# Optimization experiments

Measured on AMD Instinct MI355X. Metric: run time of the kernel, lower is better.

The kernel has to match this reference:

```python
import jax, jax.numpy as jnp
import numpy as np

B, S, D, A, C, TT, T, NS = 64, 512, 1024, 128, 64, 32, 40, 64
NEG = -1e9


def setup_inputs() -> dict:
    key = jax.random.key(0)
    ks = jax.random.split(key, 24)
    n = lambda k, sh, s: jax.random.normal(k, sh, dtype=jnp.float32) * s
    inp = {
        "encoded_src": n(ks[0], (B, S, D), 1.0),
        "encoded_col": n(ks[1], (B, C, D), 1.0),
        "encoded_tab": n(ks[2], (B, TT, D), 1.0),
        "h0": n(ks[3], (B, D), 1.0),
        "c0": n(ks[4], (B, D), 1.0),
        "action_emb": n(ks[5], (A, D), 0.1),
        "symbol_emb": n(ks[6], (NS, D), 0.1),
        "W_tgt": n(ks[7], (D, D), 0.02), "b_tgt": jnp.zeros((D,), jnp.float32),
        "W_act": n(ks[8], (D, D), 0.02), "b_act": jnp.zeros((D,), jnp.float32),
        "W_col": n(ks[9], (D, D), 0.02), "b_col": jnp.zeros((D,), jnp.float32),
        "W_tab": n(ks[10], (D, D), 0.02), "b_tab": jnp.zeros((D,), jnp.float32),
        "W_out": n(ks[11], (D, D), 0.02), "b_out": jnp.zeros((D,), jnp.float32),
        "W_ih": n(ks[12], (3 * D, 4 * D), 0.02), "b_ih": jnp.zeros((4 * D,), jnp.float32),
        "W_hh": n(ks[13], (D, 4 * D), 0.02), "b_hh": jnp.zeros((4 * D,), jnp.float32),
        "src_mask": jnp.zeros((B, S), jnp.int32),
        "col_mask": jnp.zeros((B, C), jnp.int32),
        "tab_mask": jnp.zeros((B, TT), jnp.int32),
        "action_mask": jnp.zeros((B, A), jnp.int32),
        "cur_node_ids": jax.random.randint(ks[14], (T, B), 0, NS, dtype=jnp.int32),
        "kind": jax.random.randint(ks[15], (T, B), 0, 3, dtype=jnp.int32),
        "gold_idx": jax.random.randint(ks[16], (T, B), 0, TT, dtype=jnp.int32),
    }
    return inp


def reference(encoded_src, encoded_col, encoded_tab, h0, c0, action_emb, symbol_emb,
              W_tgt, b_tgt, W_act, b_act, W_col, b_col, W_tab, b_tab, W_out, b_out,
              W_ih, b_ih, W_hh, b_hh,
              src_mask, col_mask, tab_mask, action_mask, cur_node_ids, kind, gold_idx):
    dt = encoded_src.dtype
    nT, nB = cur_node_ids.shape
    nA = action_emb.shape[0]
    nC = encoded_col.shape[1]
    nTT = encoded_tab.shape[1]
    dim = encoded_src.shape[-1]

    # mask==1 means masked-out (matches torch code: allowed positions set to 0)
    src_bias = jnp.where(src_mask == 1, NEG, 0.0).astype(dt)
    act_bias = jnp.where(action_mask == 1, NEG, 0.0).astype(dt)
    col_bias = jnp.where(col_mask == 1, NEG, 0.0).astype(dt)
    tab_bias = jnp.where(tab_mask == 1, NEG, 0.0).astype(dt)

    # previous-action embedding per step: gather from action table / encoded cols / encoded tabs
    bidx = jnp.arange(nB)
    prev_a = action_emb[gold_idx % nA]                       # [T,B,D]
    prev_c = encoded_col[bidx[None, :], gold_idx % nC]       # [T,B,D]
    prev_t = encoded_tab[bidx[None, :], gold_idx % nTT]      # [T,B,D]
    k3 = kind[..., None]
    prev_sel = jnp.where(k3 == 0, prev_a, jnp.where(k3 == 1, prev_c, prev_t))
    # step 0 uses a zero prev-action embedding
    prev_emb = jnp.concatenate([jnp.zeros((1, nB, dim), dt), prev_sel[:-1]], axis=0)
    node_emb = symbol_emb[cur_node_ids]                      # [T,B,D]

    def step(carry, xs):
        h, c, loss = carry
        pe, ne, kd, gi = xs
        # attention over encoded_src using affine(h) as query
        q = h @ W_tgt + b_tgt                                            # [B,D]
        att = jax.nn.softmax(jnp.einsum('bsd,bd->bs', encoded_src, q) + src_bias, axis=-1)
        ctx = jnp.einsum('bs,bsd->bd', att, encoded_src)                 # [B,D]
        # LSTMCell
        x = jnp.concatenate([pe, ne, ctx], axis=-1)                      # [B,3D]
        gates = x @ W_ih + b_ih + h @ W_hh + b_hh                        # [B,4D]
        i, f, g, o = jnp.split(gates, 4, axis=-1)
        c2 = jax.nn.sigmoid(f) * c + jax.nn.sigmoid(i) * jnp.tanh(g)
        h2 = jax.nn.sigmoid(o) * jnp.tanh(c2)
        out = h2 @ W_out + b_out                                         # [B,D]
        # three prediction heads (action / column / table views)
        la = jax.nn.log_softmax(jnp.einsum('ad,bd->ba', action_emb, out @ W_act + b_act) + act_bias, axis=-1)
        lc = jax.nn.log_softmax(jnp.einsum('bcd,bd->bc', encoded_col, out @ W_col + b_col) + col_bias, axis=-1)
        lt = jax.nn.log_softmax(jnp.einsum('btd,bd->bt', encoded_tab, out @ W_tab + b_tab) + tab_bias, axis=-1)
        ga = jnp.take_along_axis(la, (gi % nA)[:, None], 1)[:, 0]
        gc = jnp.take_along_axis(lc, (gi % nC)[:, None], 1)[:, 0]
        gt = jnp.take_along_axis(lt, (gi % nTT)[:, None], 1)[:, 0]
        lp = jnp.where(kd == 0, ga, jnp.where(kd == 1, gc, gt))
        return (h2, c2, loss - lp), None

    (h, c, loss), _ = jax.lax.scan(step, (h0, c0, jnp.zeros((nB,), dt)),
                                   (prev_emb, node_emb, kind, gold_idx))
    return loss
```

## Files before the change

kernel.cpp:

```cpp
#include <hip/hip_runtime.h>
#include <math.h>

typedef short s8v __attribute__((ext_vector_type(8)));
typedef __bf16 bf8 __attribute__((ext_vector_type(8)));
typedef float f4v __attribute__((ext_vector_type(4)));

#define DEV static __device__ __forceinline__

DEV ushort f2bf(float f){
  union { float f; unsigned u; } v; v.f = f;
  unsigned u = v.u;
  return (ushort)((u + 0x7fffu + ((u>>16)&1u)) >> 16);
}
DEV float bf2f(ushort u){
  union { unsigned u; float f; } v; v.u = ((unsigned)u)<<16; return v.f;
}
DEV float sigm(float x){ return 1.0f/(1.0f + __expf(-x)); }
DEV float tanh_(float x){ float e=__expf(2.f*x); return 1.f - 2.f/(e+1.f); }
DEV float wred(float x){
  #pragma unroll
  for(int off=32; off; off>>=1) x += __shfl_xor(x, off, 64);
  return x;
}
DEV int swz(int row, int uscol){
  return (row<<6) + ((((uscol>>3) ^ (row&7))<<3) | (uscol&7));
}
DEV void gload16(const void* g, void* l){
  __builtin_amdgcn_global_load_lds((const __attribute__((address_space(1))) void*)g,
                                   (__attribute__((address_space(3))) void*)l, 16, 0, 0);
}
DEV int gperm(int n){
  return (((n&1023)>>4)<<6) | ((n>>10)<<4) | (n&15);
}


__global__ void k_cast(const float* __restrict__ s, ushort* __restrict__ d, long n4){
  long i = (long)blockIdx.x*256 + threadIdx.x;
  const long st = (long)gridDim.x*256;
  for(; i<n4; i+=st){
    float4 v = ((const float4*)s)[i];
    ushort4 o; o.x=f2bf(v.x); o.y=f2bf(v.y); o.z=f2bf(v.z); o.w=f2bf(v.w);
    ((ushort4*)d)[i]=o;
  }
}

__global__ __launch_bounds__(256) void k_tr7(const float* __restrict__ wih,
    const float* __restrict__ whh, const float* __restrict__ wtgt,
    const float* __restrict__ wcol, const float* __restrict__ wtab,
    const float* __restrict__ wact, ushort* __restrict__ WihT,
    ushort* __restrict__ WcatT, ushort* __restrict__ WtgtT, ushort* __restrict__ BcatT)
{
  __shared__ ushort T[64][72];
  const int bid = blockIdx.x;
  const float* src; ushort* dst; int C, ldd, roff, cx, ry; bool pm;
  if(bid < 2048){ src=wih; C=4096; dst=WihT; ldd=2048; roff=0; cx=bid&63; ry=bid>>6; pm=true; }
  else if(bid < 3072){ int j=bid-2048; src=wih+2048L*4096; C=4096; dst=WcatT; ldd=2048; roff=0; cx=j&63; ry=j>>6; pm=true; }
  else if(bid < 4096){ int j=bid-3072; src=whh; C=4096; dst=WcatT; ldd=2048; roff=1024; cx=j&63; ry=j>>6; pm=true; }
  else if(bid < 4352){ int j=bid-4096; src=wtgt; C=1024; dst=WtgtT; ldd=1024; roff=0; cx=j&15; ry=j>>4; pm=false; }
  else if(bid < 4608){ int j=bid-4352; src=wcol; C=1024; dst=BcatT; ldd=1024; roff=0; cx=j&15; ry=j>>4; pm=false; }
  else if(bid < 4864){ int j=bid-4608; src=wtab; C=1024; dst=BcatT+1048576; ldd=1024; roff=0; cx=j&15; ry=j>>4; pm=false; }
  else { int j=bid-4864; src=wact; C=1024; dst=BcatT+2097152; ldd=1024; roff=0; cx=j&15; ry=j>>4; pm=false; }
  const int c0 = cx<<6, r0 = ry<<6;
  const int tid = threadIdx.x;
  {
    const int rr = tid>>2, cc = (tid&3)<<4;
    const float* s = src + (long)(r0+rr)*C + c0 + cc;
    float4 v0=*(const float4*)(s), v1=*(const float4*)(s+4), v2=*(const float4*)(s+8), v3=*(const float4*)(s+12);
    ushort* t = &T[rr][cc];
    t[0]=f2bf(v0.x); t[1]=f2bf(v0.y); t[2]=f2bf(v0.z); t[3]=f2bf(v0.w);
    t[4]=f2bf(v1.x); t[5]=f2bf(v1.y); t[6]=f2bf(v1.z); t[7]=f2bf(v1.w);
    t[8]=f2bf(v2.x); t[9]=f2bf(v2.y); t[10]=f2bf(v2.z); t[11]=f2bf(v2.w);
    t[12]=f2bf(v3.x); t[13]=f2bf(v3.y); t[14]=f2bf(v3.z); t[15]=f2bf(v3.w);
  }
  __syncthreads();
  {
    const int rr = tid>>2, cc = (tid&3)<<4;
    s8v o0, o1;
    #pragma unroll
    for(int i=0;i<8;i++){ o0[i]=(short)T[cc+i][rr]; o1[i]=(short)T[cc+8+i][rr]; }
    const int n = c0 + rr;
    const int nr = pm ? gperm(n) : n;
    ushort* dp = dst + (long)nr*ldd + roff + r0 + cc;
    *(s8v*)dp = o0; *(s8v*)(dp+8) = o1;
  }
}

__global__ void k_gatherP(const float* __restrict__ emba, const float* __restrict__ ecol,
                          const float* __restrict__ etab, const float* __restrict__ symb,
                          const int* __restrict__ kindv, const int* __restrict__ gold,
                          const int* __restrict__ cur, ushort* __restrict__ P){
  long i = (long)blockIdx.x*256 + threadIdx.x;
  const long st = (long)gridDim.x*256;
  const long n4 = 2560L*2048/4;
  for(; i<n4; i+=st){
    long pos = i*4; int row = (int)(pos>>11); int col = (int)(pos&2047);
    int t = row>>6, b = row&63;
    ushort4 o;
    if(col < 1024){
      if(t==0){ o.x=o.y=o.z=o.w=0; *(ushort4*)&P[pos]=o; continue; }
      int k = kindv[(t-1)*64+b];
      int gi = gold[(t-1)*64+b];
      const float* s;
      if(k==0) s = emba + ((long)(gi & 127))*1024 + col;
      else if(k==1) s = ecol + (((long)b<<6) + (gi & 63))*1024 + col;
      else s = etab + (((long)b<<5) + (gi & 31))*1024 + col;
      float4 v = *(const float4*)s;
      o.x=f2bf(v.x); o.y=f2bf(v.y); o.z=f2bf(v.z); o.w=f2bf(v.w);
    } else {
      const float* s = symb + ((long)cur[t*64+b])*1024 + (col-1024);
      float4 v = *(const float4*)s;
      o.x=f2bf(v.x); o.y=f2bf(v.y); o.z=f2bf(v.z); o.w=f2bf(v.w);
    }
    *(ushort4*)&P[pos] = o;
  }
}

__global__ void k_init(const float* __restrict__ h0, const float* __restrict__ c0,
                       const float* __restrict__ bih, const float* __restrict__ bhh,
                       const int* __restrict__ smask,
                       float* __restrict__ cbuf, ushort* __restrict__ Ab0,
                       float* __restrict__ biasvec, float* __restrict__ sbias){
  int i = blockIdx.x*256 + threadIdx.x;
  if(i < 65536){
    cbuf[i]=c0[i];
    int row=i>>10, col=i&1023;
    Ab0[(row<<11)+1024+col]=f2bf(h0[i]);
  }
  if(i < 32768) sbias[i] = (smask[i]==1) ? -1.0e9f : 0.f;
  if(i < 4096){
    int nt=i>>6, g=(i>>4)&3, j16=i&15;
    int n = (g<<10) | (nt<<4) | j16;
    biasvec[i] = bih[n] + bhh[n];
  }
}

__global__ void k_bias1(const float* __restrict__ bout,
                        const float* __restrict__ Wa, const float* __restrict__ ba,
                        const float* __restrict__ Wc, const float* __restrict__ bc,
                        const float* __restrict__ Wt, const float* __restrict__ bt,
                        float* __restrict__ vv){
  int j = blockIdx.x*256 + threadIdx.x;
  if(j >= 3072) return;
  int which = j>>10, col = j&1023;
  const float* W = (which==0)?Wa:(which==1)?Wc:Wt;
  const float* bb = (which==0)?ba:(which==1)?bc:bt;
  float s = bb[col];
  for(int i=0;i<1024;i++) s += bout[i]*W[((long)i<<10)+col];
  vv[j] = s;
}

__global__ void k_bias2a(const float* __restrict__ vv, const float* __restrict__ emb,
                         const float* __restrict__ ecol, const float* __restrict__ etab,
                         float* __restrict__ dbuf){
  int wid = blockIdx.x*4 + (threadIdx.x>>6);
  int l = threadIdx.x & 63;
  if(wid >= 6272) return;
  const float* src; const float* v;
  if(wid < 128){ src = emb + ((long)wid<<10); v = vv; }
  else if(wid < 4224){ src = ecol + ((long)(wid-128)<<10); v = vv+1024; }
  else { src = etab + ((long)(wid-4224)<<10); v = vv+2048; }
  const float* sp = src + l*16; const float* vp = v + l*16;
  float s = 0.f;
  #pragma unroll
  for(int i=0;i<16;i+=4){
    float4 a = *(const float4*)(sp+i); float4 bvv = *(const float4*)(vp+i);
    s += a.x*bvv.x + a.y*bvv.y + a.z*bvv.z + a.w*bvv.w;
  }
  s = wred(s);
  if(l==0) dbuf[wid] = s;
}

__global__ void k_bias2b(const float* __restrict__ dbuf,
                         const int* __restrict__ amask, const int* __restrict__ cmask,
                         const int* __restrict__ tmask,
                         float* __restrict__ ca, float* __restrict__ cb, float* __restrict__ ct){
  int i = blockIdx.x*256 + threadIdx.x;
  if(i < 8192){ ca[i] = dbuf[i&127] + ((amask[i]==1)?-1.0e9f:0.f); }
  else if(i < 12288){ int j=i-8192; cb[j] = dbuf[128+j] + ((cmask[j]==1)?-1.0e9f:0.f); }
  else if(i < 14336){ int j=i-12288; ct[j] = dbuf[4224+j] + ((tmask[j]==1)?-1.0e9f:0.f); }
}

template<bool OBF16, bool HASB>
__global__ __launch_bounds__(256,2) void k_gemm128(const ushort* __restrict__ Ap,
    const ushort* __restrict__ Bp, void* __restrict__ Cp, const float* __restrict__ bias,
    int N, int K)
{
  __shared__ __align__(16) ushort As[2][8192];
  __shared__ __align__(16) ushort Bs[2][8192];
  const int tid=threadIdx.x, w=tid>>6, l=tid&63;
  const int wr=w>>1, wc=w&1;
  const int m0=blockIdx.y<<7, n0=blockIdx.x<<7;
  const int lr8 = l>>3, lc = l&7;
  f4v acc[4][4];
  #pragma unroll
  for(int m=0;m<4;m++)
    #pragma unroll
    for(int n=0;n<4;n++) acc[m][n]=(f4v){0.f,0.f,0.f,0.f};

  auto stage=[&](int buf, int k0){
    #pragma unroll
    for(int i=0;i<4;i++){
      const int rb = i*32 + w*8;
      const int row = rb + lr8;
      const int cp = (lc ^ (row&7))<<3;
      gload16(Ap + (long)(m0+row)*K + k0 + cp, &As[buf][rb<<6]);
      gload16(Bp + (long)(n0+row)*K + k0 + cp, &Bs[buf][rb<<6]);
    }
  };
  auto compute=[&](int buf){
    #pragma unroll
    for(int ks=0; ks<2; ks++){
      bf8 av[4], bv[4];
      #pragma unroll
      for(int m=0;m<4;m++){
        const int ar = wr*64 + (m<<4) + (l&15);
        const int ch = (ks<<2) + (l>>4);
        av[m] = *(const bf8*)&As[buf][(ar<<6) + ((ch ^ (ar&7))<<3)];
      }
      #pragma unroll
      for(int n=0;n<4;n++){
        const int br = wc*64 + (n<<4) + (l&15);
        const int ch = (ks<<2) + (l>>4);
        bv[n] = *(const bf8*)&Bs[buf][(br<<6) + ((ch ^ (br&7))<<3)];
      }
      #pragma unroll
      for(int m=0;m<4;m++)
        #pragma unroll
        for(int n=0;n<4;n++)
          acc[m][n] = __builtin_amdgcn_mfma_f32_16x16x32_bf16(av[m], bv[n], acc[m][n], 0,0,0);
    }
  };

  stage(0, 0);
  asm volatile("s_waitcnt vmcnt(0)" ::: "memory");
  __syncthreads();
  int cur=0;
  for(int k0=0;;){
    const int kn = k0+64;
    if(kn<K) stage(cur^1, kn);
    compute(cur);
    asm volatile("s_waitcnt vmcnt(0)" ::: "memory");
    __syncthreads();
    if(kn>=K) break;
    k0=kn; cur^=1;
  }
  #pragma unroll
  for(int m=0;m<4;m++){
    #pragma unroll
    for(int n=0;n<4;n++){
      const int col = n0 + wc*64 + (n<<4) + (l&15);
      float bv_ = 0.f;
      if constexpr(HASB) bv_ = bias[col];
      #pragma unroll
      for(int j=0;j<4;j++){
        const int row = m0 + wr*64 + (m<<4) + ((l>>4)<<2) + j;
        float v = acc[m][n][j] + bv_;
        if constexpr(OBF16) ((ushort*)Cp)[(long)row*N + col] = f2bf(v);
        else ((float*)Cp)[(long)row*N + col] = v;
      }
    }
  }
}

template<bool AF32, bool OBF16, bool HASB>
__global__ __launch_bounds__(256) void k_gemm(const void* __restrict__ Ap,
    const ushort* __restrict__ Bp, void* __restrict__ Cp, const float* __restrict__ bias,
    int M, int N, int K, int lda, int ldb, int ldc, long sAz, long sCz)
{
  __shared__ __align__(16) ushort As[4096];
  __shared__ __align__(16) ushort Bs[4096];
  const int tid=threadIdx.x, w=tid>>6, l=tid&63, q4=l>>4;
  const int r=tid>>2, cc=(tid&3)<<4;
  const int m0=blockIdx.y<<6, n0=blockIdx.x<<6;
  const int z=blockIdx.z;
  f4v acc[4];
  #pragma unroll
  for(int i=0;i<4;i++) acc[i]=(f4v){0.f,0.f,0.f,0.f};

  struct PF { float4 f0,f1,f2,f3; s8v u0,u1,b0,b1; };
  PF pA, pB;

  auto loadAB=[&](int k0, PF& p){
    const int gm = m0 + r;
    if constexpr(AF32){
      if(gm < M){
        const float* a = (const float*)Ap + sAz*z + (long)gm*lda + k0 + cc;
        p.f0=*(const float4*)(a); p.f1=*(const float4*)(a+4); p.f2=*(const float4*)(a+8); p.f3=*(const float4*)(a+12);
      } else { p.f0=p.f1=p.f2=p.f3=make_float4(0.f,0.f,0.f,0.f); }
    } else {
      if(gm < M){
        const ushort* a = (const ushort*)Ap + sAz*z + (long)gm*lda + k0 + cc;
        p.u0=*(const s8v*)a; p.u1=*(const s8v*)(a+8);
      } else { p.u0=p.u1=(s8v){0,0,0,0,0,0,0,0}; }
    }
    const ushort* b = Bp + (long)(n0+r)*ldb + k0 + cc;
    p.b0=*(const s8v*)b; p.b1=*(const s8v*)(b+8);
  };
  auto stage=[&](const PF& p){
    s8v a0, a1;
    if constexpr(AF32){
      a0[0]=(short)f2bf(p.f0.x); a0[1]=(short)f2bf(p.f0.y); a0[2]=(short)f2bf(p.f0.z); a0[3]=(short)f2bf(p.f0.w);
      a0[4]=(short)f2bf(p.f1.x); a0[5]=(short)f2bf(p.f1.y); a0[6]=(short)f2bf(p.f1.z); a0[7]=(short)f2bf(p.f1.w);
      a1[0]=(short)f2bf(p.f2.x); a1[1]=(short)f2bf(p.f2.y); a1[2]=(short)f2bf(p.f2.z); a1[3]=(short)f2bf(p.f2.w);
      a1[4]=(short)f2bf(p.f3.x); a1[5]=(short)f2bf(p.f3.y); a1[6]=(short)f2bf(p.f3.z); a1[7]=(short)f2bf(p.f3.w);
    } else { a0=p.u0; a1=p.u1; }
    *(s8v*)&As[swz(r,cc)] = a0; *(s8v*)&As[swz(r,cc+8)] = a1;
    *(s8v*)&Bs[swz(r,cc)] = p.b0; *(s8v*)&Bs[swz(r,cc+8)] = p.b1;
  };
  auto compute=[&](){
    #pragma unroll
    for(int ks=0; ks<64; ks+=32){
      bf8 av = *(const bf8*)&As[swz((w<<4)+(l&15), ks+(q4<<3))];
      #pragma unroll
      for(int nf=0; nf<4; nf++){
        bf8 bv = *(const bf8*)&Bs[swz((nf<<4)+(l&15), ks+(q4<<3))];
        acc[nf] = __builtin_amdgcn_mfma_f32_16x16x32_bf16(av, bv, acc[nf], 0, 0, 0);
      }
    }
  };

  loadAB(0, pA); loadAB(64, pB);
  for(int k0=0; k0<K; k0+=128){
    stage(pA); __syncthreads();
    if(k0+128 < K) loadAB(k0+128, pA);
    compute(); __syncthreads();
    stage(pB); __syncthreads();
    if(k0+192 < K) loadAB(k0+192, pB);
    compute(); __syncthreads();
  }
  #pragma unroll
  for(int nf=0; nf<4; nf++){
    const int col = n0 + (nf<<4) + (l&15);
    float bv = 0.f;
    if constexpr(HASB) bv = bias[col];
    #pragma unroll
    for(int j=0;j<4;j++){
      const int row = m0 + (w<<4) + ((l>>4)<<2) + j;
      if(row < M){
        float v = acc[nf][j] + bv;
        if constexpr(OBF16) ((ushort*)Cp)[sCz*z + (long)row*ldc + col] = f2bf(v);
        else ((float*)Cp)[sCz*z + (long)row*ldc + col] = v;
      }
    }
  }
}


__global__ __launch_bounds__(256) void k_attn(const ushort* __restrict__ esrc,
    const float* __restrict__ q, const float* __restrict__ sbias,
    float* __restrict__ pm, float* __restrict__ pl, float* __restrict__ pctx)
{
  const int b = blockIdx.x>>4, j = blockIdx.x&15;
  const int tid = threadIdx.x, w = tid>>6, l = tid&63;
  __shared__ float ms[4], ls[4];
  __shared__ float ctxs[4][1024];
  float qr[16];
  {
    const float* qp = q + (b<<10) + (l<<4);
    #pragma unroll
    for(int i=0;i<16;i+=4){ float4 v=*(const float4*)(qp+i); qr[i]=v.x; qr[i+1]=v.y; qr[i+2]=v.z; qr[i+3]=v.w; }
  }
  float m = -3.4e38f, lsum = 0.f;
  float cacc[16];
  #pragma unroll
  for(int i=0;i<16;i++) cacc[i]=0.f;
  const int sbase = (j<<5) + w;
  for(int rr=0; rr<8; rr++){
    const int s = sbase + (rr<<2);
    const ushort* ep = esrc + (((long)((b<<9) + s))<<10) + (l<<4);
    s8v e0 = *(const s8v*)ep, e1 = *(const s8v*)(ep+8);
    float ef[16];
    #pragma unroll
    for(int i=0;i<8;i++){ ef[i]=bf2f((ushort)e0[i]); ef[8+i]=bf2f((ushort)e1[i]); }
    float d = 0.f;
    #pragma unroll
    for(int i=0;i<16;i++) d += ef[i]*qr[i];
    d = wred(d);
    d += sbias[(b<<9)+s];
    const float mn = fmaxf(m, d);
    const float sc = __expf(m - mn);
    const float p = __expf(d - mn);
    lsum = lsum*sc + p;
    #pragma unroll
    for(int i=0;i<16;i++) cacc[i] = cacc[i]*sc + p*ef[i];
    m = mn;
  }
  if(l==0){ ms[w]=m; ls[w]=lsum; }
  #pragma unroll
  for(int i=0;i<16;i++) ctxs[w][(l<<4)+i]=cacc[i];
  __syncthreads();
  const float mb = fmaxf(fmaxf(ms[0],ms[1]),fmaxf(ms[2],ms[3]));
  const float w0=__expf(ms[0]-mb), w1=__expf(ms[1]-mb), w2=__expf(ms[2]-mb), w3=__expf(ms[3]-mb);
  const float lb = ls[0]*w0 + ls[1]*w1 + ls[2]*w2 + ls[3]*w3;
  const int jb = (j<<6) + b;
  float* pc = pctx + ((long)jb<<10);
  for(int d0=tid; d0<1024; d0+=256){
    pc[d0] = ctxs[0][d0]*w0 + ctxs[1][d0]*w1 + ctxs[2][d0]*w2 + ctxs[3][d0]*w3;
  }
  if(tid==0){ pm[jb]=mb; pl[jb]=lb; }
}

__global__ __launch_bounds__(256) void k_combine(const float* __restrict__ pm,
    const float* __restrict__ pl, const float* __restrict__ pctx, ushort* __restrict__ Ab)
{
  const int idx = blockIdx.x*256 + threadIdx.x;
  const int b = idx>>7, c0 = (idx&127)<<3;
  float mv[16];
  #pragma unroll
  for(int j=0;j<16;j++) mv[j] = pm[(j<<6)+b];
  float M = mv[0];
  #pragma unroll
  for(int j=1;j<16;j++) M = fmaxf(M, mv[j]);
  float e[16]; float den = 0.f;
  #pragma unroll
  for(int j=0;j<16;j++){ e[j] = __expf(mv[j]-M); den += pl[(j<<6)+b]*e[j]; }
  const float inv = 1.f/den;
  float s0=0,s1=0,s2=0,s3=0,s4=0,s5=0,s6=0,s7=0;
  #pragma unroll
  for(int j=0;j<16;j++){
    const float wj = e[j]*inv;
    const float* p = pctx + (((long)((j<<6)+b))<<10) + c0;
    float4 v0=*(const float4*)p, v1=*(const float4*)(p+4);
    s0+=wj*v0.x; s1+=wj*v0.y; s2+=wj*v0.z; s3+=wj*v0.w;
    s4+=wj*v1.x; s5+=wj*v1.y; s6+=wj*v1.z; s7+=wj*v1.w;
  }
  s8v o;
  o[0]=(short)f2bf(s0); o[1]=(short)f2bf(s1); o[2]=(short)f2bf(s2); o[3]=(short)f2bf(s3);
  o[4]=(short)f2bf(s4); o[5]=(short)f2bf(s5); o[6]=(short)f2bf(s6); o[7]=(short)f2bf(s7);
  *(s8v*)&Ab[(b<<11)+c0] = o;
}

__global__ __launch_bounds__(256) void k_lstm(const ushort* __restrict__ Abuf,
    const float* __restrict__ cin, const ushort* __restrict__ WcatP,
    const ushort* __restrict__ gpre_t, float* __restrict__ cout,
    ushort* __restrict__ AbOut, ushort* __restrict__ h2t)
{
  __shared__ __align__(16) ushort As[4096];
  __shared__ __align__(16) ushort Bs[4096];
  const int tid=threadIdx.x, w=tid>>6, l=tid&63, q4=l>>4, l15=l&15;
  const int r=tid>>2, cc=(tid&3)<<4;
  const int nt = blockIdx.x;
  f4v acc[4];
  #pragma unroll
  for(int nf=0;nf<4;nf++){
    #pragma unroll
    for(int jj=0;jj<4;jj++){
      const int row = (w<<4) + ((l>>4)<<2) + jj;
      acc[nf][jj] = bf2f(gpre_t[((long)row<<12) + (nt<<6) + (nf<<4) + l15]);
    }
  }
  struct PF { s8v a0,a1,b0,b1; };
  PF pA, pB;
  auto loadAB=[&](int k0, PF& p){
    const ushort* a = Abuf + ((long)r<<11) + k0 + cc;
    p.a0=*(const s8v*)a; p.a1=*(const s8v*)(a+8);
    const ushort* bp = WcatP + ((long)((nt<<6)+r)<<11) + k0 + cc;
    p.b0=*(const s8v*)bp; p.b1=*(const s8v*)(bp+8);
  };
  auto stage=[&](const PF& p){
    *(s8v*)&As[swz(r,cc)] = p.a0; *(s8v*)&As[swz(r,cc+8)] = p.a1;
    *(s8v*)&Bs[swz(r,cc)] = p.b0; *(s8v*)&Bs[swz(r,cc+8)] = p.b1;
  };
  auto compute=[&](){
    #pragma unroll
    for(int ks=0; ks<64; ks+=32){
      bf8 av = *(const bf8*)&As[swz((w<<4)+l15, ks+(q4<<3))];
      #pragma unroll
      for(int nf=0;nf<4;nf++){
        bf8 bv = *(const bf8*)&Bs[swz((nf<<4)+l15, ks+(q4<<3))];
        acc[nf] = __builtin_amdgcn_mfma_f32_16x16x32_bf16(av, bv, acc[nf], 0, 0, 0);
      }
    }
  };
  loadAB(0, pA); loadAB(64, pB);
  for(int k0=0; k0<2048; k0+=128){
    stage(pA); __syncthreads();
    if(k0+128 < 2048) loadAB(k0+128, pA);
    compute(); __syncthreads();
    stage(pB); __syncthreads();
    if(k0+192 < 2048) loadAB(k0+192, pB);
    compute(); __syncthreads();
  }
  #pragma unroll
  for(int jj=0;jj<4;jj++){
    const int row = (w<<4) + ((l>>4)<<2) + jj;
    const int j = (nt<<4) + l15;
    const float iv = acc[0][jj], fv = acc[1][jj], gv = acc[2][jj], ov = acc[3][jj];
    const float cold = cin[(row<<10)+j];
    const float c2 = sigm(fv)*cold + sigm(iv)*tanh_(gv);
    const float h2v = sigm(ov)*tanh_(c2);
    cout[(row<<10)+j] = c2;
    const ushort hb = f2bf(h2v);
    AbOut[(row<<11) + 1024 + j] = hb;
    h2t[(row<<10)+j] = hb;
  }
}

__global__ __launch_bounds__(256) void k_loss(const ushort* __restrict__ h2a,
    const ushort* __restrict__ GAt, const ushort* __restrict__ GCt, const ushort* __restrict__ GTt,
    const float* __restrict__ ca, const float* __restrict__ cb, const float* __restrict__ ct,
    const int* __restrict__ gold, const int* __restrict__ kindv, float* __restrict__ lossbuf)
{
  const int blk = blockIdx.x;
  const int t = blk/192, rem = blk - t*192;
  const int b = rem/3, head = rem - b*3;
  const int tid = threadIdx.x, w = tid>>6, l = tid&63;
  __shared__ float logits[128];
  int R; const ushort* G; const float* cons;
  if(head==0){ R=128; G=GAt; cons=ca + (b<<7); }
  else if(head==1){ R=64; G=GCt + ((long)b<<16); cons=cb + (b<<6); }
  else { R=32; G=GTt + ((long)b<<15); cons=ct + (b<<5); }
  float hr[16];
  {
    const ushort* hp = h2a + (((long)((t<<6)+b))<<10) + l*16;
    s8v h0v=*(const s8v*)hp, h1v=*(const s8v*)(hp+8);
    #pragma unroll
    for(int i=0;i<8;i++){ hr[i]=bf2f((ushort)h0v[i]); hr[8+i]=bf2f((ushort)h1v[i]); }
  }
  for(int rr=w; rr<R; rr+=4){
    const ushort* gp = G + ((long)rr<<10) + l*16;
    s8v g0=*(const s8v*)gp, g1=*(const s8v*)(gp+8);
    float d = 0.f;
    #pragma unroll
    for(int i=0;i<8;i++){ d += bf2f((ushort)g0[i])*hr[i]; d += bf2f((ushort)g1[i])*hr[8+i]; }
    d = wred(d);
    if(l==0) logits[rr] = d + cons[rr];
  }
  __syncthreads();
  if(w==0){
    float mx = -3.4e38f;
    for(int idx=l; idx<R; idx+=64) mx = fmaxf(mx, logits[idx]);
    #pragma unroll
    for(int off=32; off; off>>=1) mx = fmaxf(mx, __shfl_xor(mx, off, 64));
    float s = 0.f;
    for(int idx=l; idx<R; idx+=64) s += __expf(logits[idx]-mx);
    s = wred(s);
    if(l==0){
      const float lse = mx + __logf(s);
      const int kd = kindv[(t<<6)+b];
      const bool mine = (head==0 && kd==0) || (head==1 && kd==1) || (head==2 && kd>=2);
      if(mine){
        const int gi = gold[(t<<6)+b];
        lossbuf[(t<<6)+b] = logits[gi & (R-1)] - lse;
      }
    }
  }
}

__global__ void k_loss_fin(const float* __restrict__ lossbuf, float* __restrict__ out){
  int b = threadIdx.x;
  if(b < 64){
    float s = 0.f;
    for(int t=0;t<40;t++) s += lossbuf[(t<<6)+b];
    out[b] = -s;
  }
}


extern "C" void kernel_launch(void* const* d_in, const int* in_sizes, int n_in,
                              void* d_out, int out_size, void* d_ws, size_t ws_size,
                              hipStream_t stream)
{
  const float *e_src=(const float*)d_in[0], *e_col=(const float*)d_in[1], *e_tab=(const float*)d_in[2];
  const float *h0=(const float*)d_in[3], *c0=(const float*)d_in[4];
  const float *emba=(const float*)d_in[5], *embs=(const float*)d_in[6];
  const float *W_tgt=(const float*)d_in[7], *b_tgt=(const float*)d_in[8];
  const float *W_act=(const float*)d_in[9], *b_act=(const float*)d_in[10];
  const float *W_col=(const float*)d_in[11], *b_col=(const float*)d_in[12];
  const float *W_tab=(const float*)d_in[13], *b_tab=(const float*)d_in[14];
  const float *W_out=(const float*)d_in[15], *b_out=(const float*)d_in[16];
  const float *W_ih=(const float*)d_in[17], *b_ih=(const float*)d_in[18];
  const float *W_hh=(const float*)d_in[19], *b_hh=(const float*)d_in[20];
  const int *smask=(const int*)d_in[21], *cmask=(const int*)d_in[22], *tmask=(const int*)d_in[23];
  const int *amask=(const int*)d_in[24];
  const int *cur=(const int*)d_in[25], *kindp=(const int*)d_in[26], *goldp=(const int*)d_in[27];

  char* wp = (char*)d_ws;
  auto alloc = [&](size_t n)->char*{ char* p = wp; wp += (n + 255) & ~(size_t)255; return p; };
  ushort* esrc_bf = (ushort*)alloc(67108864);
  ushort* WihT    = (ushort*)alloc(16777216);
  ushort* WcatP   = (ushort*)alloc(16777216);
  ushort* WtgtT   = (ushort*)alloc(2097152);
  ushort* BcatT   = (ushort*)alloc(6291456);
  ushort* Woutb   = (ushort*)alloc(2097152);
  float*  U       = (float*) alloc(12582912);
  ushort* Ubf     = (ushort*)alloc(6291456);
  ushort* GAt     = (ushort*)alloc(262144);
  ushort* GCt     = (ushort*)alloc(8388608);
  ushort* GTt     = (ushort*)alloc(4194304);
  ushort* gpre    = (ushort*)alloc(20971520);
  float* biasvec  = (float*)alloc(16384);
  float* sbias    = (float*)alloc(131072);
  float* vv       = (float*)alloc(12288);
  float* dbuf     = (float*)alloc(25088);
  float* ca       = (float*)alloc(32768);
  float* cb       = (float*)alloc(16384);
  float* ctb      = (float*)alloc(8192);
  float* pm       = (float*)alloc(4096);
  float* pl       = (float*)alloc(4096);
  float* pctx     = (float*)alloc(4194304);
  ushort* Ab0     = (ushort*)alloc(262144);
  ushort* Ab1     = (ushort*)alloc(262144);
  float* cbuf0    = (float*)alloc(262144);
  float* cbuf1    = (float*)alloc(262144);
  float* qb       = (float*)alloc(262144);
  ushort* h2a     = (ushort*)alloc(5242880);
  float* lossbuf  = (float*)alloc(10240);
  ushort* P       = (ushort*)U;
  float* out      = (float*)d_out;

  k_cast<<<4096,256,0,stream>>>(e_src, esrc_bf, 8388608L);
  k_cast<<<512,256,0,stream>>>(W_out, Woutb, 262144L);
  k_tr7<<<5120,256,0,stream>>>(W_ih, W_hh, W_tgt, W_col, W_tab, W_act,
                               WihT, WcatP, WtgtT, BcatT);
  k_init<<<256,256,0,stream>>>(h0, c0, b_ih, b_hh, smask, cbuf0, Ab0, biasvec, sbias);

  { dim3 g(24,8); k_gemm128<false,false><<<g,256,0,stream>>>(Woutb, BcatT, U, nullptr, 3072, 1024); }
  k_cast<<<1024,256,0,stream>>>(U, Ubf, 786432L);
  { dim3 g(16,2); k_gemm<true,true,false><<<g,256,0,stream>>>(emba, Ubf+2048, GAt, nullptr,
        128,1024,1024, 1024,3072,1024, 0,0); }
  { dim3 g(16,1,64); k_gemm<true,true,false><<<g,256,0,stream>>>(e_col, Ubf, GCt, nullptr,
        64,1024,1024, 1024,3072,1024, 65536,65536); }
  { dim3 g(16,1,64); k_gemm<true,true,false><<<g,256,0,stream>>>(e_tab, Ubf+1024, GTt, nullptr,
        32,1024,1024, 1024,3072,1024, 32768,32768); }
  k_bias1<<<12,256,0,stream>>>(b_out, W_act, b_act, W_col, b_col, W_tab, b_tab, vv);
  k_bias2a<<<1568,256,0,stream>>>(vv, emba, e_col, e_tab, dbuf);
  k_bias2b<<<56,256,0,stream>>>(dbuf, amask, cmask, tmask, ca, cb, ctb);

  k_gatherP<<<2048,256,0,stream>>>(emba, e_col, e_tab, embs, kindp, goldp, cur, P);
  { dim3 g(32,20); k_gemm128<true,true><<<g,256,0,stream>>>(P, WihT, gpre, biasvec, 4096, 2048); }
  { dim3 g(16,1); k_gemm<true,false,true><<<g,256,0,stream>>>(h0, WtgtT, qb, b_tgt,
        64,1024,1024, 1024,1024,1024, 0,0); }

  for(int t=0; t<40; t++){
    ushort* Ain  = (t&1) ? Ab1 : Ab0;
    ushort* Aout = (t&1) ? Ab0 : Ab1;
    float* ci = (t&1) ? cbuf1 : cbuf0;
    float* co = (t&1) ? cbuf0 : cbuf1;
    k_attn<<<1024,256,0,stream>>>(esrc_bf, qb, sbias, pm, pl, pctx);
    k_combine<<<32,256,0,stream>>>(pm, pl, pctx, Ain);
    k_lstm<<<64,256,0,stream>>>(Ain, ci, WcatP, gpre + (long)t*262144, co, Aout, h2a + (long)t*65536);
    { dim3 g(16,1); k_gemm<false,false,true><<<g,256,0,stream>>>(Aout + 1024, WtgtT, qb, b_tgt,
          64,1024,1024, 2048,1024,1024, 0,0); }
  }
  k_loss<<<7680,256,0,stream>>>(h2a, GAt, GCt, GTt, ca, cb, ctb, goldp, kindp, lossbuf);
  k_loss_fin<<<1,64,0,stream>>>(lossbuf, out);
}
```

Baseline: 2.140 ms.

## Replace per-step LSTM and loss kernels with pipelined small GEMMs and batched logit GEMMs

```diff
diff --git a/kernel.cpp b/kernel.cpp
--- a/kernel.cpp
+++ b/kernel.cpp
@@ -189,7 +189,11 @@
   __shared__ __align__(16) ushort Bs[2][8192];
   const int tid=threadIdx.x, w=tid>>6, l=tid&63;
   const int wr=w>>1, wc=w&1;
-  const int m0=blockIdx.y<<7, n0=blockIdx.x<<7;
+  const int nwg = gridDim.x*gridDim.y;
+  const int orig = blockIdx.y*gridDim.x + blockIdx.x;
+  const int xcd = orig & 7, qq = nwg>>3, rr_ = nwg&7;
+  const int wgid = (xcd<rr_ ? xcd*(qq+1) : rr_*(qq+1)+(xcd-rr_)*qq) + (orig>>3);
+  const int m0 = (wgid / gridDim.x)<<7, n0 = (wgid % gridDim.x)<<7;
   const int lr8 = l>>3, lc = l&7;
   f4v acc[4][4];
   #pragma unroll
@@ -265,7 +269,7 @@
 template<bool AF32, bool OBF16, bool HASB>
 __global__ __launch_bounds__(256) void k_gemm(const void* __restrict__ Ap,
     const ushort* __restrict__ Bp, void* __restrict__ Cp, const float* __restrict__ bias,
-    int M, int N, int K, int lda, int ldb, int ldc, long sAz, long sCz)
+    int M, int N, int K, int lda, int ldb, int ldc, long sAz, long sBz, long sCz)
 {
   __shared__ __align__(16) ushort As[4096];
   __shared__ __align__(16) ushort Bs[4096];
@@ -293,7 +297,7 @@
         p.u0=*(const s8v*)a; p.u1=*(const s8v*)(a+8);
       } else { p.u0=p.u1=(s8v){0,0,0,0,0,0,0,0}; }
     }
-    const ushort* b = Bp + (long)(n0+r)*ldb + k0 + cc;
+    const ushort* b = Bp + sBz*z + (long)(n0+r)*ldb + k0 + cc;
     p.b0=*(const s8v*)b; p.b1=*(const s8v*)(b+8);
   };
   auto stage=[&](const PF& p){
@@ -345,6 +349,98 @@
   }
 }
 
+template<int EPI>
+__global__ __launch_bounds__(256) void k_sgemm(
+    const ushort* __restrict__ Ap, int lda,
+    const ushort* __restrict__ Bp, int ldb, int K,
+    const ushort* __restrict__ gpre_t, const float* __restrict__ cin,
+    float* __restrict__ cout, ushort* __restrict__ AbOut, ushort* __restrict__ h2t,
+    const float* __restrict__ btgt, float* __restrict__ qout)
+{
+  __shared__ __align__(16) ushort As[2][4096];
+  __shared__ __align__(16) ushort Bs[2][4096];
+  const int tid=threadIdx.x, w=tid>>6, l=tid&63, l15=l&15;
+  const int lr8=l>>3, lc=l&7;
+  const int nt=blockIdx.x;
+  f4v acc[4];
+  if constexpr(EPI==1){
+    #pragma unroll
+    for(int nf=0;nf<4;nf++){
+      #pragma unroll
+      for(int jj=0;jj<4;jj++){
+        const int row=(w<<4)+((l>>4)<<2)+jj;
+        acc[nf][jj]=bf2f(gpre_t[((long)row<<12)+(nt<<6)+(nf<<4)+l15]);
+      }
+    }
+  } else {
+    #pragma unroll
+    for(int i=0;i<4;i++) acc[i]=(f4v){0.f,0.f,0.f,0.f};
+  }
+  auto stage=[&](int buf,int k0){
+    #pragma unroll
+    for(int i=0;i<2;i++){
+      const int rb=i*32+w*8;
+      const int row=rb+lr8;
+      const int cp=(lc^(row&7))<<3;
+      gload16(Ap + (long)row*lda + k0 + cp, &As[buf][rb<<6]);
+      gload16(Bp + (long)((nt<<6)+row)*ldb + k0 + cp, &Bs[buf][rb<<6]);
+    }
+  };
+  auto compute=[&](int buf){
+    #pragma unroll
+    for(int ks=0;ks<2;ks++){
+      const int ch=(ks<<2)+(l>>4);
+      const int ar=(w<<4)+l15;
+      bf8 av = *(const bf8*)&As[buf][(ar<<6)+((ch^(ar&7))<<3)];
+      #pragma unroll
+      for(int nf=0;nf<4;nf++){
+        const int br=(nf<<4)+l15;
+        bf8 bv = *(const bf8*)&Bs[buf][(br<<6)+((ch^(br&7))<<3)];
+        acc[nf]=__builtin_amdgcn_mfma_f32_16x16x32_bf16(av,bv,acc[nf],0,0,0);
+      }
+    }
+  };
+  stage(0,0);
+  asm volatile("s_waitcnt vmcnt(0)" ::: "memory");
+  __syncthreads();
+  int cur=0;
+  for(int k0=0;;){
+    const int kn=k0+64;
+    if(kn<K) stage(cur^1,kn);
+    compute(cur);
+    asm volatile("s_waitcnt vmcnt(0)" ::: "memory");
+    __syncthreads();
+    if(kn>=K) break;
+    k0=kn; cur^=1;
+  }
+  if constexpr(EPI==1){
+    #pragma unroll
+    for(int jj=0;jj<4;jj++){
+      const int row=(w<<4)+((l>>4)<<2)+jj;
+      const int j=(nt<<4)+l15;
+      const float iv=acc[0][jj], fv=acc[1][jj], gv=acc[2][jj], ov=acc[3][jj];
+      const float cold=cin[(row<<10)+j];
+      const float c2=sigm(fv)*cold + sigm(iv)*tanh_(gv);
+      const float h2v=sigm(ov)*tanh_(c2);
+      cout[(row<<10)+j]=c2;
+      const ushort hb=f2bf(h2v);
+      AbOut[(row<<11)+1024+j]=hb;
+      h2t[(row<<10)+j]=hb;
+    }
+  } else {
+    #pragma unroll
+    for(int nf=0;nf<4;nf++){
+      const int col=(nt<<6)+(nf<<4)+l15;
+      const float bv=btgt[col];
+      #pragma unroll
+      for(int jj=0;jj<4;jj++){
+        const int row=(w<<4)+((l>>4)<<2)+jj;
+        qout[(row<<10)+col]=acc[nf][jj]+bv;
+      }
+    }
+  }
+}
+
 
 __global__ __launch_bounds__(256) void k_attn(const ushort* __restrict__ esrc,
     const float* __restrict__ q, const float* __restrict__ sbias,
@@ -430,121 +526,30 @@
   *(s8v*)&Ab[(b<<11)+c0] = o;
 }
 
-__global__ __launch_bounds__(256) void k_lstm(const ushort* __restrict__ Abuf,
-    const float* __restrict__ cin, const ushort* __restrict__ WcatP,
-    const ushort* __restrict__ gpre_t, float* __restrict__ cout,
-    ushort* __restrict__ AbOut, ushort* __restrict__ h2t)
-{
-  __shared__ __align__(16) ushort As[4096];
-  __shared__ __align__(16) ushort Bs[4096];
-  const int tid=threadIdx.x, w=tid>>6, l=tid&63, q4=l>>4, l15=l&15;
-  const int r=tid>>2, cc=(tid&3)<<4;
-  const int nt = blockIdx.x;
-  f4v acc[4];
-  #pragma unroll
-  for(int nf=0;nf<4;nf++){
-    #pragma unroll
-    for(int jj=0;jj<4;jj++){
-      const int row = (w<<4) + ((l>>4)<<2) + jj;
-      acc[nf][jj] = bf2f(gpre_t[((long)row<<12) + (nt<<6) + (nf<<4) + l15]);
-    }
-  }
-  struct PF { s8v a0,a1,b0,b1; };
-  PF pA, pB;
-  auto loadAB=[&](int k0, PF& p){
-    const ushort* a = Abuf + ((long)r<<11) + k0 + cc;
-    p.a0=*(const s8v*)a; p.a1=*(const s8v*)(a+8);
-    const ushort* bp = WcatP + ((long)((nt<<6)+r)<<11) + k0 + cc;
-    p.b0=*(const s8v*)bp; p.b1=*(const s8v*)(bp+8);
-  };
-  auto stage=[&](const PF& p){
-    *(s8v*)&As[swz(r,cc)] = p.a0; *(s8v*)&As[swz(r,cc+8)] = p.a1;
-    *(s8v*)&Bs[swz(r,cc)] = p.b0; *(s8v*)&Bs[swz(r,cc+8)] = p.b1;
-  };
-  auto compute=[&](){
-    #pragma unroll
-    for(int ks=0; ks<64; ks+=32){
-      bf8 av = *(const bf8*)&As[swz((w<<4)+l15, ks+(q4<<3))];
-      #pragma unroll
-      for(int nf=0;nf<4;nf++){
-        bf8 bv = *(const bf8*)&Bs[swz((nf<<4)+l15, ks+(q4<<3))];
-        acc[nf] = __builtin_amdgcn_mfma_f32_16x16x32_bf16(av, bv, acc[nf], 0, 0, 0);
-      }
-    }
-  };
-  loadAB(0, pA); loadAB(64, pB);
-  for(int k0=0; k0<2048; k0+=128){
-    stage(pA); __syncthreads();
-    if(k0+128 < 2048) loadAB(k0+128, pA);
-    compute(); __syncthreads();
-    stage(pB); __syncthreads();
-    if(k0+192 < 2048) loadAB(k0+192, pB);
-    compute(); __syncthreads();
-  }
-  #pragma unroll
-  for(int jj=0;jj<4;jj++){
-    const int row = (w<<4) + ((l>>4)<<2) + jj;
-    const int j = (nt<<4) + l15;
-    const float iv = acc[0][jj], fv = acc[1][jj], gv = acc[2][jj], ov = acc[3][jj];
-    const float cold = cin[(row<<10)+j];
-    const float c2 = sigm(fv)*cold + sigm(iv)*tanh_(gv);
-    const float h2v = sigm(ov)*tanh_(c2);
-    cout[(row<<10)+j] = c2;
-    const ushort hb = f2bf(h2v);
-    AbOut[(row<<11) + 1024 + j] = hb;
-    h2t[(row<<10)+j] = hb;
-  }
-}
-
-__global__ __launch_bounds__(256) void k_loss(const ushort* __restrict__ h2a,
-    const ushort* __restrict__ GAt, const ushort* __restrict__ GCt, const ushort* __restrict__ GTt,
+__global__ __launch_bounds__(256) void k_loss2(const float* __restrict__ la,
+    const float* __restrict__ lcb, const float* __restrict__ ltb,
     const float* __restrict__ ca, const float* __restrict__ cb, const float* __restrict__ ct,
     const int* __restrict__ gold, const int* __restrict__ kindv, float* __restrict__ lossbuf)
 {
-  const int blk = blockIdx.x;
-  const int t = blk/192, rem = blk - t*192;
-  const int b = rem/3, head = rem - b*3;
-  const int tid = threadIdx.x, w = tid>>6, l = tid&63;
-  __shared__ float logits[128];
-  int R; const ushort* G; const float* cons;
-  if(head==0){ R=128; G=GAt; cons=ca + (b<<7); }
-  else if(head==1){ R=64; G=GCt + ((long)b<<16); cons=cb + (b<<6); }
-  else { R=32; G=GTt + ((long)b<<15); cons=ct + (b<<5); }
-  float hr[16];
-  {
-    const ushort* hp = h2a + (((long)((t<<6)+b))<<10) + l*16;
-    s8v h0v=*(const s8v*)hp, h1v=*(const s8v*)(hp+8);
-    #pragma unroll
-    for(int i=0;i<8;i++){ hr[i]=bf2f((ushort)h0v[i]); hr[8+i]=bf2f((ushort)h1v[i]); }
-  }
-  for(int rr=w; rr<R; rr+=4){
-    const ushort* gp = G + ((long)rr<<10) + l*16;
-    s8v g0=*(const s8v*)gp, g1=*(const s8v*)(gp+8);
-    float d = 0.f;
-    #pragma unroll
-    for(int i=0;i<8;i++){ d += bf2f((ushort)g0[i])*hr[i]; d += bf2f((ushort)g1[i])*hr[8+i]; }
-    d = wred(d);
-    if(l==0) logits[rr] = d + cons[rr];
-  }
-  __syncthreads();
-  if(w==0){
-    float mx = -3.4e38f;
-    for(int idx=l; idx<R; idx+=64) mx = fmaxf(mx, logits[idx]);
-    #pragma unroll
-    for(int off=32; off; off>>=1) mx = fmaxf(mx, __shfl_xor(mx, off, 64));
-    float s = 0.f;
-    for(int idx=l; idx<R; idx+=64) s += __expf(logits[idx]-mx);
-    s = wred(s);
-    if(l==0){
-      const float lse = mx + __logf(s);
-      const int kd = kindv[(t<<6)+b];
-      const bool mine = (head==0 && kd==0) || (head==1 && kd==1) || (head==2 && kd>=2);
-      if(mine){
-        const int gi = gold[(t<<6)+b];
-        lossbuf[(t<<6)+b] = logits[gi & (R-1)] - lse;
-      }
-    }
-  }
+  const int wv = threadIdx.x>>6, l = threadIdx.x&63;
+  const int tb = blockIdx.x*4 + wv;
+  const int t = tb>>6, b = tb&63;
+  const int kd = kindv[tb];
+  const int gi = gold[tb];
+  const float* ptr; const float* cons; int R;
+  if(kd==0){ ptr = la + (long)tb*128; cons = ca + (b<<7); R=128; }
+  else if(kd==1){ ptr = lcb + (long)b*2560 + t*64; cons = cb + (b<<6); R=64; }
+  else { ptr = ltb + (long)b*2560 + t*64; cons = ct + (b<<5); R=32; }
+  const int gidx = gi & (R-1);
+  const float v  = (l < R) ? (ptr[l] + cons[l]) : -3.4e38f;
+  const float v2 = (R==128) ? (ptr[l+64] + cons[l+64]) : -3.4e38f;
+  float mx = fmaxf(v, v2);
+  #pragma unroll
+  for(int off=32; off; off>>=1) mx = fmaxf(mx, __shfl_xor(mx, off, 64));
+  float s = ((l<R)?__expf(v-mx):0.f) + ((R==128)?__expf(v2-mx):0.f);
+  s = wred(s);
+  const float gv = ptr[gidx] + cons[gidx];
+  if(l==0) lossbuf[tb] = gv - (mx + __logf(s));
 }
 
 __global__ void k_loss_fin(const float* __restrict__ lossbuf, float* __restrict__ out){
@@ -587,7 +592,7 @@
   ushort* Ubf     = (ushort*)alloc(6291456);
   ushort* GAt     = (ushort*)alloc(262144);
   ushort* GCt     = (ushort*)alloc(8388608);
-  ushort* GTt     = (ushort*)alloc(4194304);
+  ushort* GTt     = (ushort*)alloc(8388608);
   ushort* gpre    = (ushort*)alloc(20971520);
   float* biasvec  = (float*)alloc(16384);
   float* sbias    = (float*)alloc(131072);
@@ -605,6 +610,9 @@
   float* cbuf1    = (float*)alloc(262144);
   float* qb       = (float*)alloc(262144);
   ushort* h2a     = (ushort*)alloc(5242880);
+  float* la       = (float*)alloc(1310720);
+  float* lcb      = (float*)alloc(655360);
+  float* ltb      = (float*)alloc(655360);
   float* lossbuf  = (float*)alloc(10240);
   ushort* P       = (ushort*)U;
   float* out      = (float*)d_out;
@@ -618,19 +626,19 @@
   { dim3 g(24,8); k_gemm128<false,false><<<g,256,0,stream>>>(Woutb, BcatT, U, nullptr, 3072, 1024); }
   k_cast<<<1024,256,0,stream>>>(U, Ubf, 786432L);
   { dim3 g(16,2); k_gemm<true,true,false><<<g,256,0,stream>>>(emba, Ubf+2048, GAt, nullptr,
-        128,1024,1024, 1024,3072,1024, 0,0); }
+        128,1024,1024, 1024,3072,1024, 0,0,0); }
   { dim3 g(16,1,64); k_gemm<true,true,false><<<g,256,0,stream>>>(e_col, Ubf, GCt, nullptr,
-        64,1024,1024, 1024,3072,1024, 65536,65536); }
+        64,1024,1024, 1024,3072,1024, 65536,0,65536); }
   { dim3 g(16,1,64); k_gemm<true,true,false><<<g,256,0,stream>>>(e_tab, Ubf+1024, GTt, nullptr,
-        32,1024,1024, 1024,3072,1024, 32768,32768); }
+        32,1024,1024, 1024,3072,1024, 32768,0,65536); }
   k_bias1<<<12,256,0,stream>>>(b_out, W_act, b_act, W_col, b_col, W_tab, b_tab, vv);
   k_bias2a<<<1568,256,0,stream>>>(vv, emba, e_col, e_tab, dbuf);
   k_bias2b<<<56,256,0,stream>>>(dbuf, amask, cmask, tmask, ca, cb, ctb);
 
   k_gatherP<<<2048,256,0,stream>>>(emba, e_col, e_tab, embs, kindp, goldp, cur, P);
   { dim3 g(32,20); k_gemm128<true,true><<<g,256,0,stream>>>(P, WihT, gpre, biasvec, 4096, 2048); }
-  { dim3 g(16,1); k_gemm<true,false,true><<<g,256,0,stream>>>(h0, WtgtT, qb, b_tgt,
-        64,1024,1024, 1024,1024,1024, 0,0); }
+  k_sgemm<0><<<16,256,0,stream>>>(Ab0+1024, 2048, WtgtT, 1024, 1024,
+        nullptr, nullptr, nullptr, nullptr, nullptr, b_tgt, qb);
 
   for(int t=0; t<40; t++){
     ushort* Ain  = (t&1) ? Ab1 : Ab0;
@@ -639,10 +647,17 @@
     float* co = (t&1) ? cbuf0 : cbuf1;
     k_attn<<<1024,256,0,stream>>>(esrc_bf, qb, sbias, pm, pl, pctx);
     k_combine<<<32,256,0,stream>>>(pm, pl, pctx, Ain);
-    k_lstm<<<64,256,0,stream>>>(Ain, ci, WcatP, gpre + (long)t*262144, co, Aout, h2a + (long)t*65536);
-    { dim3 g(16,1); k_gemm<false,false,true><<<g,256,0,stream>>>(Aout + 1024, WtgtT, qb, b_tgt,
-          64,1024,1024, 2048,1024,1024, 0,0); }
-  }
-  k_loss<<<7680,256,0,stream>>>(h2a, GAt, GCt, GTt, ca, cb, ctb, goldp, kindp, lossbuf);
+    k_sgemm<1><<<64,256,0,stream>>>(Ain, 2048, WcatP, 2048, 2048,
+        gpre + (long)t*262144, ci, co, Aout, h2a + (long)t*65536, nullptr, nullptr);
+    k_sgemm<0><<<16,256,0,stream>>>(Aout+1024, 2048, WtgtT, 1024, 1024,
+        nullptr, nullptr, nullptr, nullptr, nullptr, b_tgt, qb);
+  }
+
+  { dim3 g(1,20); k_gemm128<false,false><<<g,256,0,stream>>>(h2a, GAt, la, nullptr, 128, 1024); }
+  { dim3 g(1,1,64); k_gemm<false,false,false><<<g,256,0,stream>>>(h2a, GCt, lcb, nullptr,
+        40,64,1024, 65536,1024,64, 1024,65536,2560); }
+  { dim3 g(1,1,64); k_gemm<false,false,false><<<g,256,0,stream>>>(h2a, GTt, ltb, nullptr,
+        40,64,1024, 65536,1024,64, 1024,65536,2560); }
+  k_loss2<<<640,256,0,stream>>>(la, lcb, ltb, ca, cb, ctb, goldp, kindp, lossbuf);
   k_loss_fin<<<1,64,0,stream>>>(lossbuf, out);
 }
```

New measurement: 2.393 ms. 11.8% more time.
